# Performance work log

Measured on AMD Instinct MI355X. Metric: run time of the kernel, lower is better.

The kernel has to match this reference:

```python
import jax, jax.numpy as jnp
import numpy as np

N = 10000
E = 160000
NT = 4      # num_types
NB = 8      # bessel basis size
U = 32      # env_embed_multiplicity
R_MAX = 6.0
AVG_NEIGH = 16.0
POLY_P = 6.0


def _mlp(x, Ws):
    # nequip ScalarMLPFunction: no biases, forward-normalized weights, SiLU between layers
    n = len(Ws)
    for i, W in enumerate(Ws):
        x = x @ (W * (1.0 / jnp.sqrt(jnp.float32(W.shape[0]))))
        if i < n - 1:
            x = jax.nn.silu(x)
    return x


def _poly_cutoff(r, rc, p=POLY_P):
    x = r / rc
    out = (1.0 - ((p + 1.0) * (p + 2.0) / 2.0) * x ** p
           + p * (p + 2.0) * x ** (p + 1.0)
           - (p * (p + 1.0) / 2.0) * x ** (p + 2.0))
    return out * (x < 1.0)


def _weighted_channels(edge_attr, w):
    # MakeWeightedChannels: per-edge, per-channel weight for each irrep block
    # edge_attr: [E,4] = (0e | 1o), w: [E,U,2] -> out [E,U,4]
    wd = jnp.concatenate([w[:, :, 0:1], jnp.repeat(w[:, :, 1:2], 3, axis=-1)], axis=-1)
    return edge_attr[:, None, :] * wd


def _forward(edge_index, node_attrs, edge_attr, edge_embed, edge_length,
             W2b0, W2b1, W2b2, Wenv0, Wlat0, Wlat1, Wenv1, Wfin0, Wfin1,
             Wlin_s, Wlin_v, resnet_params):
    n_nodes = node_attrs.shape[0]
    n_edges = edge_attr.shape[0]
    center, neigh = edge_index[0], edge_index[1]
    cut = _poly_cutoff(edge_length, R_MAX)[:, None]           # [E,1], same per-layer cutoff
    env_norm = 1.0 / jnp.sqrt(AVG_NEIGH)
    sqrt3 = jnp.sqrt(3.0)
    c = jnp.exp(resnet_params)                                 # resnet update coefficients

    # ---- two-body latent (layer 0 latent)
    lat_in = jnp.concatenate([node_attrs[center], node_attrs[neigh], edge_embed], axis=-1)
    latents = _mlp(lat_in, [W2b0, W2b1, W2b2]) * cut           # [E,512]
    norm2 = c[0] ** 2
    latents = latents * (c[0] / jnp.sqrt(norm2))

    # env-embed MLP layer 0: feature weights + env weights
    w0 = _mlp(latents, [Wenv0])                                # [E,4U]
    w_feat = w0[:, :2 * U].reshape(n_edges, U, 2)
    w_env = w0[:, 2 * U:].reshape(n_edges, U, 2)
    features = _weighted_channels(edge_attr, w_feat)           # [E,U,4]

    def env_embed_edges(w_env):
        env_w = _weighted_channels(edge_attr, w_env)           # [E,U,4]
        env = jax.ops.segment_sum(env_w, center, num_segments=n_nodes) * env_norm
        return env[center]                                     # [E,U,4]

    # ---- layer 0 TP ('uuu', e3nn component norm): (0e+1o) x (0e+1o) -> [0e,0e,1o,1o]
    env_e = env_embed_edges(w_env)
    t0 = features[:, :, 0] * env_e[:, :, 0]
    t1 = jnp.sum(features[:, :, 1:] * env_e[:, :, 1:], axis=-1) / sqrt3
    v0 = features[:, :, 0:1] * env_e[:, :, 1:]
    v1 = features[:, :, 1:] * env_e[:, :, 0:1]
    scalars = jnp.concatenate([t0, t1], axis=-1)               # [E,2U]
    # e3nn Linear mixing full_out_irreps back to (0e+1o) x U
    alpha = 1.0 / jnp.sqrt(2.0 * U)
    y_s = (scalars @ Wlin_s) * alpha                           # [E,U]
    x_v = jnp.concatenate([v0, v1], axis=1)                    # [E,2U,3]
    y_v = jnp.einsum('ekd,ko->eod', x_v, Wlin_v) * alpha       # [E,U,3]
    features = jnp.concatenate([y_s[..., None], y_v], axis=-1)

    # latent resnet update
    new_lat = _mlp(jnp.concatenate([latents, scalars], axis=-1), [Wlat0, Wlat1]) * cut
    latents = (jnp.sqrt(norm2) * latents + c[1] * new_lat) / jnp.sqrt(norm2 + c[1] ** 2)
    norm2 = norm2 + c[1] ** 2

    w_env = _mlp(latents, [Wenv1]).reshape(n_edges, U, 2)

    # ---- layer 1 TP (last layer): only scalar outputs [0e,0e]
    env_e = env_embed_edges(w_env)
    t0 = features[:, :, 0] * env_e[:, :, 0]
    t1 = jnp.sum(features[:, :, 1:] * env_e[:, :, 1:], axis=-1) / sqrt3
    scalars = jnp.concatenate([t0, t1], axis=-1)               # [E,2U]
    # (the last-layer Linear output features are never used downstream -> skipped)

    # ---- final latent
    new_lat = _mlp(jnp.concatenate([latents, scalars], axis=-1), [Wfin0, Wfin1]) * cut
    latents = (jnp.sqrt(norm2) * latents + c[2] * new_lat) / jnp.sqrt(norm2 + c[2] ** 2)
    return latents                                             # [E,512] edge features


def setup_inputs() -> dict:
    key = jax.random.key(0)
    ks = jax.random.split(key, 20)
    edge_index = jax.random.randint(ks[0], (2, E), 0, N)
    node_types = jax.random.randint(ks[1], (N,), 0, NT)
    node_attrs = jax.nn.one_hot(node_types, NT, dtype=jnp.float32)
    edge_length = jax.random.uniform(ks[2], (E,), minval=0.5, maxval=R_MAX)
    vec = jax.random.normal(ks[3], (E, 3), dtype=jnp.float32)
    unit = vec / jnp.linalg.norm(vec, axis=-1, keepdims=True)
    # component-normalized real spherical harmonics: l=0 -> 1, l=1 -> sqrt(3)*unit
    edge_attr = jnp.concatenate([jnp.ones((E, 1), jnp.float32), jnp.sqrt(3.0) * unit], axis=-1)
    nb = jnp.arange(1, NB + 1, dtype=jnp.float32)
    edge_embed = (jnp.sqrt(2.0 / R_MAX)
                  * jnp.sin(nb[None, :] * jnp.pi * edge_length[:, None] / R_MAX)
                  / edge_length[:, None])
    w = lambda k, shp: jax.random.normal(k, shp, dtype=jnp.float32)
    return {
        'edge_index': edge_index, 'node_attrs': node_attrs, 'edge_attr': edge_attr,
        'edge_embed': edge_embed, 'edge_length': edge_length,
        'W2b0': w(ks[4], (2 * NT + NB, 128)), 'W2b1': w(ks[5], (128, 256)), 'W2b2': w(ks[6], (256, 512)),
        'Wenv0': w(ks[7], (512, 4 * U)),
        'Wlat0': w(ks[8], (512 + 2 * U, 512)), 'Wlat1': w(ks[9], (512, 512)),
        'Wenv1': w(ks[10], (512, 2 * U)),
        'Wfin0': w(ks[11], (512 + 2 * U, 512)), 'Wfin1': w(ks[12], (512, 512)),
        'Wlin_s': w(ks[13], (2 * U, U)), 'Wlin_v': w(ks[14], (2 * U, U)),
        'resnet_params': jnp.zeros((3,), jnp.float32),
    }


def reference(edge_index, node_attrs, edge_attr, edge_embed, edge_length,
              W2b0, W2b1, W2b2, Wenv0, Wlat0, Wlat1, Wenv1, Wfin0, Wfin1,
              Wlin_s, Wlin_v, resnet_params):
    return _forward(edge_index, node_attrs, edge_attr, edge_embed, edge_length,
                    W2b0, W2b1, W2b2, Wenv0, Wlat0, Wlat1, Wenv1, Wfin0, Wfin1,
                    Wlin_s, Wlin_v, resnet_params)
```

## Files before the change

### kernel.cpp

```cpp
#include <hip/hip_runtime.h>
#include <math.h>

#define E_EDGES 160000
#define N_NODES 10000

typedef __attribute__((ext_vector_type(8))) __bf16 bf16x8;
typedef __attribute__((ext_vector_type(4))) float f32x4;
typedef __attribute__((ext_vector_type(4))) unsigned int u32x4;

__device__ __forceinline__ unsigned short f2bf(float x) {
    unsigned u = __float_as_uint(x);
    u += 0x7fff + ((u >> 16) & 1);
    return (unsigned short)(u >> 16);
}
__device__ __forceinline__ float bf2f(unsigned short h) {
    return __uint_as_float(((unsigned)h) << 16);
}
__device__ __forceinline__ float siluf(float v) {
    return v / (1.0f + __expf(-v));
}
__device__ __forceinline__ void gload16(const unsigned short* g, unsigned short* l) {
    __builtin_amdgcn_global_load_lds(
        (const __attribute__((address_space(1))) void*)g,
        (__attribute__((address_space(3))) void*)l, 16, 0, 0);
}

__global__ __launch_bounds__(256)
void prep_kernel(const int* __restrict__ ei, const float* __restrict__ na,
                 const float* __restrict__ embed, const float* __restrict__ elen,
                 float* __restrict__ cut, unsigned short* __restrict__ A16b,
                 int* __restrict__ deg)
{
    int e = blockIdx.x * blockDim.x + threadIdx.x;
    if (e >= E_EDGES) return;
    float r  = elen[e];
    float x  = r * (1.0f / 6.0f);
    float x2 = x * x;
    float x6 = x2 * x2 * x2;
    float c = 1.0f - 28.0f * x6 + 48.0f * x6 * x - 21.0f * x6 * x2;
    cut[e] = (x < 1.0f) ? c : 0.0f;
    int ctr = ei[e];
    int ngh = ei[E_EDGES + e];
    atomicAdd(&deg[ctr], 1);
    float4 ac = *(const float4*)(na + (size_t)ctr * 4);
    float4 an = *(const float4*)(na + (size_t)ngh * 4);
    float4 b0 = *(const float4*)(embed + (size_t)e * 8);
    float4 b1 = *(const float4*)(embed + (size_t)e * 8 + 4);
    unsigned short* o = A16b + (size_t)e * 32;
    o[0]  = f2bf(ac.x); o[1]  = f2bf(ac.y); o[2]  = f2bf(ac.z); o[3]  = f2bf(ac.w);
    o[4]  = f2bf(an.x); o[5]  = f2bf(an.y); o[6]  = f2bf(an.z); o[7]  = f2bf(an.w);
    o[8]  = f2bf(b0.x); o[9]  = f2bf(b0.y); o[10] = f2bf(b0.z); o[11] = f2bf(b0.w);
    o[12] = f2bf(b1.x); o[13] = f2bf(b1.y); o[14] = f2bf(b1.z); o[15] = f2bf(b1.w);
    #pragma unroll
    for (int i = 16; i < 32; ++i) o[i] = 0;
}

__global__ __launch_bounds__(256)
void wtrans_all(const float* __restrict__ w0, const float* __restrict__ w1,
                const float* __restrict__ w2, const float* __restrict__ w3,
                const float* __restrict__ w4, const float* __restrict__ w5,
                const float* __restrict__ w6, const float* __restrict__ w7,
                const float* __restrict__ w8, unsigned short* __restrict__ wbuf)
{
    int blk = blockIdx.x;
    const float* W; int K, N, Kpad, Npad; size_t dbase; int lstart; float sc;
    const float s16  = 0.25f;
    const float s128 = 0.088388347648318447f;
    const float s256 = 0.0625f;
    const float s512 = 0.044194173824159223f;
    const float s576 = 0.041666666666666664f;
    if      (blk <   16) { W=w0; K=16;  N=128; Kpad=32;  Npad=128; dbase=0;       lstart=0;    sc=s16;  }
    else if (blk <  144) { W=w1; K=128; N=256; Kpad=128; Npad=256; dbase=4096;    lstart=16;   sc=s128; }
    else if (blk <  656) { W=w2; K=256; N=512; Kpad=256; Npad=512; dbase=36864;   lstart=144;  sc=s256; }
    else if (blk <  912) { W=w3; K=512; N=128; Kpad=512; Npad=128; dbase=167936;  lstart=656;  sc=s512; }
    else if (blk < 2064) { W=w4; K=576; N=512; Kpad=576; Npad=512; dbase=233472;  lstart=912;  sc=s576; }
    else if (blk < 3088) { W=w5; K=512; N=512; Kpad=512; Npad=512; dbase=528384;  lstart=2064; sc=s512; }
    else if (blk < 3344) { W=w6; K=512; N=64;  Kpad=512; Npad=128; dbase=790528;  lstart=3088; sc=s512; }
    else if (blk < 4496) { W=w7; K=576; N=512; Kpad=576; Npad=512; dbase=856064;  lstart=3344; sc=s576; }
    else                 { W=w8; K=512; N=512; Kpad=512; Npad=512; dbase=1150976; lstart=4496; sc=s512; }
    int local = (blk - lstart) * 256 + threadIdx.x;
    int n = local % Npad, k = local / Npad;
    if (k >= Kpad) return;
    float v = (k < K && n < N) ? W[(size_t)k * N + n] * sc : 0.0f;
    wbuf[dbase + (size_t)n * Kpad + k] = f2bf(v);
}

__global__ __launch_bounds__(1024)
void scan_kernel(const int* __restrict__ deg, int* __restrict__ offs)
{
    __shared__ int part[1024];
    int t = threadIdx.x;
    int base = t * 10;
    int loc[10];
    int s = 0;
    #pragma unroll
    for (int i = 0; i < 10; ++i) {
        int idx = base + i;
        int d = (idx < N_NODES) ? deg[idx] : 0;
        loc[i] = s; s += d;
    }
    part[t] = s;
    __syncthreads();
    for (int o = 1; o < 1024; o <<= 1) {
        int v = (t >= o) ? part[t - o] : 0;
        __syncthreads();
        part[t] += v;
        __syncthreads();
    }
    int excl = (t > 0) ? part[t - 1] : 0;
    #pragma unroll
    for (int i = 0; i < 10; ++i) {
        int idx = base + i;
        if (idx < N_NODES) offs[idx] = excl + loc[i];
    }
    if (t == 1023) offs[N_NODES] = part[1023];
}

__global__ __launch_bounds__(256)
void fill_kernel(const int* __restrict__ ei, const int* __restrict__ offs,
                 int* __restrict__ cnt, int* __restrict__ elist)
{
    int e = blockIdx.x * blockDim.x + threadIdx.x;
    if (e >= E_EDGES) return;
    int c = ei[e];
    int pos = offs[c] + atomicAdd(&cnt[c], 1);
    elist[pos] = e;
}

__global__ __launch_bounds__(256)
void sortseg_kernel(const int* __restrict__ offs, int* __restrict__ elist)
{
    int node = blockIdx.x * 4 + (threadIdx.x >> 6);
    int l = threadIdx.x & 63;
    if (node >= N_NODES) return;
    int b = offs[node], en = offs[node + 1];
    int deg = en - b;
    if (deg <= 1) return;
    if (deg <= 64) {
        int v = (l < deg) ? elist[b + l] : 0x7fffffff;
        #pragma unroll
        for (int k = 2; k <= 64; k <<= 1) {
            #pragma unroll
            for (int j = k >> 1; j > 0; j >>= 1) {
                int o = __shfl_xor(v, j);
                bool dirUp = ((l & k) == 0);
                bool lower = ((l & j) == 0);
                int mn = v < o ? v : o;
                int mx = v < o ? o : v;
                v = (dirUp == lower) ? mn : mx;
            }
        }
        if (l < deg) elist[b + l] = v;
    } else if (l == 0) {
        for (int i = b + 1; i < en; ++i) {
            int v = elist[i];
            int j = i - 1;
            while (j >= b && elist[j] > v) { elist[j + 1] = elist[j]; --j; }
            elist[j + 1] = v;
        }
    }
}

__global__ __launch_bounds__(256)
void envgather_kernel(const unsigned short* __restrict__ Wb, int wstride, int woff,
                      const float* __restrict__ ea, const int* __restrict__ offs,
                      const int* __restrict__ elist, float* __restrict__ env)
{
    int n = blockIdx.x * 2 + (threadIdx.x >> 7);
    int t = threadIdx.x & 127;
    if (n >= N_NODES) return;
    int u = t >> 2, comp = t & 3;
    int widx = woff + u * 2 + (comp ? 1 : 0);
    int beg = offs[n], end = offs[n + 1];
    float acc = 0.0f;
    for (int i = beg; i < end; ++i) {
        int e = elist[i];
        float w = bf2f(Wb[(size_t)e * wstride + widx]);
        float a = ea[(size_t)e * 4 + comp];
        acc += a * w;
    }
    env[(size_t)n * 128 + t] = acc * 0.25f;
}

template<int EPIL>
__global__ __launch_bounds__(256)
void gemm_bf16(const unsigned short* __restrict__ A1,
               int K, const unsigned short* __restrict__ Bt,
               int nx, int ldc, int Nstore,
               unsigned short* __restrict__ Cb)
{
    __shared__ __align__(16) unsigned short SB[3][2][128 * 32];
    const int tid  = threadIdx.x;
    const int lane = tid & 63;
    const int wid  = tid >> 6;
    const int wr   = wid >> 1, wc = wid & 1;
    const int nwg = gridDim.x;
    const int fid = blockIdx.x;
    const int q = nwg >> 3, r = nwg & 7;
    const int xcd = fid & 7, j = fid >> 3;
    const int L = ((xcd < r) ? xcd * (q + 1) : r * (q + 1) + (xcd - r) * q) + j;
    const int bn = (L % nx) * 128;
    const int bm = (L / nx) * 128;

    const int l15 = lane & 15;
    const int l4r = lane >> 2;
    const int sk8 = (((lane & 3) ^ ((lane >> 3) & 3)) << 3);
    const int rk8 = ((((lane >> 4) ^ ((l15 >> 1) & 3)) & 3) << 3);
    const int T   = K >> 5;

    f32x4 acc[4][4] = {};

    auto stage = [&](int t, int b) {
        int k0 = t << 5;
        #pragma unroll
        for (int i = 0; i < 2; ++i) {
            int ch  = (wid << 1) + i;
            int row = (ch << 4) + l4r;
            gload16(A1 + (size_t)(bm + row) * K + k0 + sk8, &SB[b][0][ch << 9]);
            gload16(Bt + (size_t)(bn + row) * K + k0 + sk8, &SB[b][1][ch << 9]);
        }
    };

    stage(0, 0);
    if (T >= 2) stage(1, 1);

    for (int t = 0; t < T; ++t) {
        if (t < T - 1) asm volatile("s_waitcnt vmcnt(4)" ::: "memory");
        else           asm volatile("s_waitcnt vmcnt(0)" ::: "memory");
        __builtin_amdgcn_s_barrier();
        __builtin_amdgcn_sched_barrier(0);

        if (t + 2 < T) stage(t + 2, (t + 2) % 3);

        const unsigned short* As = &SB[t % 3][0][0];
        const unsigned short* Bs = &SB[t % 3][1][0];
        bf16x8 af[4], bfr[4];
        #pragma unroll
        for (int m = 0; m < 4; ++m)
            af[m] = __builtin_bit_cast(bf16x8, *(const u32x4*)&As[(wr * 64 + m * 16 + l15) * 32 + rk8]);
        #pragma unroll
        for (int n = 0; n < 4; ++n)
            bfr[n] = __builtin_bit_cast(bf16x8, *(const u32x4*)&Bs[(wc * 64 + n * 16 + l15) * 32 + rk8]);

        __builtin_amdgcn_s_setprio(1);
        #pragma unroll
        for (int m = 0; m < 4; ++m)
            #pragma unroll
            for (int n = 0; n < 4; ++n)
                acc[m][n] = __builtin_amdgcn_mfma_f32_16x16x32_bf16(af[m], bfr[n], acc[m][n], 0, 0, 0);
        __builtin_amdgcn_s_setprio(0);

        asm volatile("s_waitcnt lgkmcnt(0)" ::: "memory");
        __builtin_amdgcn_sched_barrier(0);
    }

    #pragma unroll
    for (int m = 0; m < 4; ++m) {
        int rbase = bm + wr * 64 + m * 16 + ((lane >> 4) << 2);
        #pragma unroll
        for (int n = 0; n < 4; ++n) {
            int col = bn + wc * 64 + n * 16 + l15;
            if (col < Nstore) {
                #pragma unroll
                for (int rr = 0; rr < 4; ++rr) {
                    int row = rbase + rr;
                    Cb[(size_t)row * ldc + col] = f2bf(acc[m][n][rr]);
                }
            }
        }
    }
}

__global__ __launch_bounds__(512)
void mlp2b(const unsigned short* __restrict__ A16b,
           const unsigned short* __restrict__ W0t,
           const unsigned short* __restrict__ W1t,
           const unsigned short* __restrict__ W2t,
           const float* __restrict__ cut, unsigned short* __restrict__ Lb)
{
    __shared__ __align__(16) unsigned short SA[64 * 32];
    __shared__ __align__(16) unsigned short H1[64 * 128];
    __shared__ __align__(16) unsigned short H2[64 * 256];
    const int tid  = threadIdx.x;
    const int lane = tid & 63;
    const int wid  = tid >> 6;
    const int l15  = lane & 15;
    const int l4r  = lane >> 2;
    const int lk8  = (lane >> 4) << 3;
    const int sk8  = (((lane & 3) ^ ((lane >> 3) & 3)) << 3);
    const int rk8  = ((((lane >> 4) ^ ((l15 >> 1) & 3)) & 3) << 3);
    const int bm   = blockIdx.x * 64;
    const int hrow4 = (lane >> 4) << 2;

    if (wid < 4) {
        int row = (wid << 4) + l4r;
        gload16(A16b + (size_t)(bm + row) * 32 + sk8, &SA[wid << 9]);
    }
    asm volatile("s_waitcnt vmcnt(0)" ::: "memory");
    __builtin_amdgcn_s_barrier();
    __builtin_amdgcn_sched_barrier(0);

    {
        int hc = wid * 16 + l15;
        bf16x8 wf = __builtin_bit_cast(bf16x8, *(const u32x4*)(W0t + (size_t)hc * 32 + lk8));
        #pragma unroll
        for (int mi = 0; mi < 4; ++mi) {
            bf16x8 af = __builtin_bit_cast(bf16x8, *(const u32x4*)&SA[(mi * 16 + l15) * 32 + rk8]);
            f32x4 a = {};
            a = __builtin_amdgcn_mfma_f32_16x16x32_bf16(af, wf, a, 0, 0, 0);
            #pragma unroll
            for (int rr = 0; rr < 4; ++rr) {
                int er = mi * 16 + hrow4 + rr;
                H1[er * 128 + (((hc >> 3) ^ (er & 7)) << 3) + (hc & 7)] = f2bf(siluf(a[rr]));
            }
        }
    }
    asm volatile("s_waitcnt lgkmcnt(0)" ::: "memory");
    __builtin_amdgcn_s_barrier();
    __builtin_amdgcn_sched_barrier(0);

    {
        f32x4 acc[4][2] = {};
        #pragma unroll
        for (int kt = 0; kt < 4; ++kt) {
            bf16x8 hf[4], wf[2];
            #pragma unroll
            for (int fa = 0; fa < 4; ++fa) {
                int er = fa * 16 + l15;
                int slotp = (kt * 4 + (lane >> 4)) ^ (er & 7);
                hf[fa] = __builtin_bit_cast(bf16x8, *(const u32x4*)&H1[er * 128 + slotp * 8]);
            }
            #pragma unroll
            for (int fb = 0; fb < 2; ++fb) {
                int hc = wid * 32 + fb * 16 + l15;
                wf[fb] = __builtin_bit_cast(bf16x8, *(const u32x4*)(W1t + (size_t)hc * 128 + kt * 32 + lk8));
            }
            #pragma unroll
            for (int fa = 0; fa < 4; ++fa)
                #pragma unroll
                for (int fb = 0; fb < 2; ++fb)
                    acc[fa][fb] = __builtin_amdgcn_mfma_f32_16x16x32_bf16(hf[fa], wf[fb], acc[fa][fb], 0, 0, 0);
        }
        asm volatile("s_waitcnt lgkmcnt(0)" ::: "memory");
        __builtin_amdgcn_s_barrier();
        #pragma unroll
        for (int fa = 0; fa < 4; ++fa)
            #pragma unroll
            for (int fb = 0; fb < 2; ++fb)
                #pragma unroll
                for (int rr = 0; rr < 4; ++rr) {
                    int er = fa * 16 + hrow4 + rr;
                    int hc = wid * 32 + fb * 16 + l15;
                    H2[er * 256 + (((hc >> 3) ^ (er & 7)) << 3) + (hc & 7)] = f2bf(siluf(acc[fa][fb][rr]));
                }
    }
    asm volatile("s_waitcnt lgkmcnt(0)" ::: "memory");
    __builtin_amdgcn_s_barrier();
    __builtin_amdgcn_sched_barrier(0);

    f32x4 acc[4][4] = {};
    #pragma unroll 1
    for (int kt = 0; kt < 8; ++kt) {
        bf16x8 hf[4], wf[4];
        #pragma unroll
        for (int fa = 0; fa < 4; ++fa) {
            int er = fa * 16 + l15;
            int slotp = (kt * 4 + (lane >> 4)) ^ (er & 7);
            hf[fa] = __builtin_bit_cast(bf16x8, *(const u32x4*)&H2[er * 256 + slotp * 8]);
        }
        #pragma unroll
        for (int fb = 0; fb < 4; ++fb) {
            int oc = wid * 64 + fb * 16 + l15;
            wf[fb] = __builtin_bit_cast(bf16x8, *(const u32x4*)(W2t + (size_t)oc * 256 + kt * 32 + lk8));
        }
        __builtin_amdgcn_s_setprio(1);
        #pragma unroll
        for (int fa = 0; fa < 4; ++fa)
            #pragma unroll
            for (int fb = 0; fb < 4; ++fb)
                acc[fa][fb] = __builtin_amdgcn_mfma_f32_16x16x32_bf16(hf[fa], wf[fb], acc[fa][fb], 0, 0, 0);
        __builtin_amdgcn_s_setprio(0);
    }
    #pragma unroll
    for (int fa = 0; fa < 4; ++fa) {
        int rbase = bm + fa * 16 + hrow4;
        #pragma unroll
        for (int fb = 0; fb < 4; ++fb) {
            int col = wid * 64 + fb * 16 + l15;
            #pragma unroll
            for (int rr = 0; rr < 4; ++rr) {
                int row = rbase + rr;
                Lb[(size_t)row * 512 + col] = f2bf(acc[fa][fb][rr] * cut[row]);
            }
        }
    }
}

template<int EPIL2>
__global__ __launch_bounds__(512)
void fused_mlp(const unsigned short* __restrict__ A1,
               const unsigned short* __restrict__ A2,
               const unsigned short* __restrict__ W1t,
               const unsigned short* __restrict__ W2t,
               float* __restrict__ Cf, unsigned short* __restrict__ Cb,
               const float* __restrict__ cut, const float* __restrict__ rp)
{
    __shared__ __align__(16) unsigned short Hl[128 * 512];
    __shared__ __align__(16) unsigned short SA[3][128 * 32];
    const int tid  = threadIdx.x;
    const int lane = tid & 63;
    const int wid  = tid >> 6;
    const int l15  = lane & 15;
    const int l4r  = lane >> 2;
    const int lk8  = (lane >> 4) << 3;
    const int sk8  = (((lane & 3) ^ ((lane >> 3) & 3)) << 3);
    const int rk8  = ((((lane >> 4) ^ ((l15 >> 1) & 3)) & 3) << 3);
    const int bm   = blockIdx.x * 128;
    const int hcol0 = wid * 64;
    const int ocol0 = wid * 64;

    auto stage = [&](int t, int b) {
        int k0 = t << 5;
        int row = (wid << 4) + l4r;
        const unsigned short* gp;
        if (k0 < 512) gp = A1 + (size_t)(bm + row) * 512 + k0 + sk8;
        else          gp = A2 + (size_t)(bm + row) * 64 + (k0 - 512) + sk8;
        gload16(gp, &SA[b][wid << 9]);
    };

    f32x4 acc1[8][4] = {};
    stage(0, 0);
    stage(1, 1);

    for (int t = 0; t < 18; ++t) {
        __builtin_amdgcn_sched_barrier(0);
        if (t < 17) asm volatile("s_waitcnt vmcnt(1)" ::: "memory");
        else        asm volatile("s_waitcnt vmcnt(0)" ::: "memory");
        __builtin_amdgcn_s_barrier();
        __builtin_amdgcn_sched_barrier(0);

        const unsigned short* As = &SA[t % 3][0];
        int k0 = t << 5;
        bf16x8 af[8], wf[4];
        #pragma unroll
        for (int mi = 0; mi < 8; ++mi)
            af[mi] = __builtin_bit_cast(bf16x8, *(const u32x4*)&As[(mi * 16 + l15) * 32 + rk8]);
        #pragma unroll
        for (int ni = 0; ni < 4; ++ni) {
            int hc = hcol0 + ni * 16 + l15;
            wf[ni] = __builtin_bit_cast(bf16x8, *(const u32x4*)(W1t + (size_t)hc * 576 + k0 + lk8));
        }
        __builtin_amdgcn_sched_barrier(0);
        if (t + 2 < 18) stage(t + 2, (t + 2) % 3);
        __builtin_amdgcn_sched_barrier(0);
        asm volatile("s_waitcnt lgkmcnt(0)" ::: "memory");
        __builtin_amdgcn_sched_barrier(0);

        __builtin_amdgcn_s_setprio(1);
        #pragma unroll
        for (int mi = 0; mi < 8; ++mi)
            #pragma unroll
            for (int ni = 0; ni < 4; ++ni)
                acc1[mi][ni] = __builtin_amdgcn_mfma_f32_16x16x32_bf16(af[mi], wf[ni], acc1[mi][ni], 0, 0, 0);
        __builtin_amdgcn_s_setprio(0);
    }

    #pragma unroll
    for (int mi = 0; mi < 8; ++mi)
        #pragma unroll
        for (int ni = 0; ni < 4; ++ni)
            #pragma unroll
            for (int rr = 0; rr < 4; ++rr) {
                int er = mi * 16 + ((lane >> 4) << 2) + rr;
                int hc = hcol0 + ni * 16 + l15;
                float v = acc1[mi][ni][rr];
                v = v / (1.0f + __expf(-v));
                int slotp = (hc >> 3) ^ (er & 7);
                Hl[er * 512 + slotp * 8 + (hc & 7)] = f2bf(v);
            }
    asm volatile("s_waitcnt lgkmcnt(0)" ::: "memory");
    __builtin_amdgcn_s_barrier();
    __builtin_amdgcn_sched_barrier(0);

    f32x4 acc2[8][4] = {};
    #pragma unroll 1
    for (int kt = 0; kt < 16; ++kt) {
        bf16x8 hf[8], w2f[4];
        #pragma unroll
        for (int fa = 0; fa < 8; ++fa) {
            int er = fa * 16 + l15;
            int slotp = (kt * 4 + (lane >> 4)) ^ (er & 7);
            hf[fa] = __builtin_bit_cast(bf16x8, *(const u32x4*)&Hl[er * 512 + slotp * 8]);
        }
        #pragma unroll
        for (int fb = 0; fb < 4; ++fb) {
            int oc = ocol0 + fb * 16 + l15;
            w2f[fb] = __builtin_bit_cast(bf16x8, *(const u32x4*)(W2t + (size_t)oc * 512 + kt * 32 + lk8));
        }
        __builtin_amdgcn_s_setprio(1);
        #pragma unroll
        for (int fa = 0; fa < 8; ++fa)
            #pragma unroll
            for (int fb = 0; fb < 4; ++fb)
                acc2[fa][fb] = __builtin_amdgcn_mfma_f32_16x16x32_bf16(hf[fa], w2f[fb], acc2[fa][fb], 0, 0, 0);
        __builtin_amdgcn_s_setprio(0);
    }

    float c0 = __expf(rp[0]), c1 = __expf(rp[1]), c2 = __expf(rp[2]);
    #pragma unroll
    for (int fa = 0; fa < 8; ++fa) {
        int rbase = bm + fa * 16 + ((lane >> 4) << 2);
        #pragma unroll
        for (int fb = 0; fb < 4; ++fb) {
            int col = ocol0 + fb * 16 + l15;
            #pragma unroll
            for (int rr = 0; rr < 4; ++rr) {
                int row = rbase + rr;
                float v = acc2[fa][fb][rr];
                size_t off2 = (size_t)row * 512 + col;
                if (EPIL2 == 3) {
                    float old = bf2f(Cb[off2]);
                    v = (c0 * old + c1 * v * cut[row]) * rsqrtf(c0 * c0 + c1 * c1);
                    Cb[off2] = f2bf(v);
                } else {
                    float old = bf2f(Cb[off2]);
                    float n2 = c0 * c0 + c1 * c1;
                    v = (sqrtf(n2) * old + c2 * v * cut[row]) * rsqrtf(n2 + c2 * c2);
                    Cf[off2] = v;
                }
            }
        }
    }
}

__global__ __launch_bounds__(256)
void tp0_kernel(const unsigned short* __restrict__ W0b, const float* __restrict__ ea,
                const float* __restrict__ env, const int* __restrict__ ei,
                const float* __restrict__ Ws, const float* __restrict__ Wv,
                unsigned short* __restrict__ scalb, unsigned short* __restrict__ feat2b)
{
    __shared__ float sc[8][64];
    __shared__ float xv[8][64][3];
    __shared__ float Wsl[2048];
    __shared__ float Wvl[2048];
    int tid = threadIdx.x;
    const float alpha = 0.125f;
    #pragma unroll
    for (int i = 0; i < 8; ++i) {
        Wsl[tid + i * 256] = Ws[tid + i * 256] * alpha;
        Wvl[tid + i * 256] = Wv[tid + i * 256] * alpha;
    }
    int le = tid >> 5;
    int u  = tid & 31;
    int e  = blockIdx.x * 8 + le;
    int c  = ei[e];
    float4 a = *(const float4*)(ea + (size_t)e * 4);
    const float* ep = env + (size_t)c * 128 + u * 4;
    float e0 = ep[0], e1 = ep[1], e2 = ep[2], e3 = ep[3];
    float wf0 = bf2f(W0b[(size_t)e * 128 + u * 2]);
    float wf1 = bf2f(W0b[(size_t)e * 128 + u * 2 + 1]);
    float f0 = a.x * wf0;
    float f1 = a.y * wf1, f2 = a.z * wf1, f3 = a.w * wf1;
    const float rs3 = 0.57735026918962576f;
    float t0 = f0 * e0;
    float t1 = (f1 * e1 + f2 * e2 + f3 * e3) * rs3;
    scalb[(size_t)e * 64 + u]      = f2bf(t0);
    scalb[(size_t)e * 64 + 32 + u] = f2bf(t1);
    sc[le][u]      = t0;
    sc[le][32 + u] = t1;
    xv[le][u][0] = f0 * e1; xv[le][u][1] = f0 * e2; xv[le][u][2] = f0 * e3;
    xv[le][32 + u][0] = f1 * e0; xv[le][32 + u][1] = f2 * e0; xv[le][32 + u][2] = f3 * e0;
    __syncthreads();
    float ys = 0.0f, yv0 = 0.0f, yv1 = 0.0f, yv2 = 0.0f;
    #pragma unroll 8
    for (int k = 0; k < 64; ++k) {
        float ws = Wsl[k * 32 + u];
        float wv = Wvl[k * 32 + u];
        ys  = fmaf(sc[le][k], ws, ys);
        yv0 = fmaf(xv[le][k][0], wv, yv0);
        yv1 = fmaf(xv[le][k][1], wv, yv1);
        yv2 = fmaf(xv[le][k][2], wv, yv2);
    }
    ushort4 ov;
    ov.x = f2bf(ys);
    ov.y = f2bf(yv0);
    ov.z = f2bf(yv1);
    ov.w = f2bf(yv2);
    *(ushort4*)(feat2b + (size_t)e * 128 + u * 4) = ov;
}

__global__ __launch_bounds__(256)
void tp1_kernel(const unsigned short* __restrict__ feat2b, const float* __restrict__ env,
                const int* __restrict__ ei, unsigned short* __restrict__ scalb)
{
    int idx = blockIdx.x * blockDim.x + threadIdx.x;
    if (idx >= E_EDGES * 32) return;
    int e = idx >> 5, u = idx & 31;
    int c = ei[e];
    const float* ep = env + (size_t)c * 128 + u * 4;
    ushort4 f4 = *(const ushort4*)(feat2b + (size_t)e * 128 + u * 4);
    float fx = bf2f(f4.x), fy = bf2f(f4.y), fz = bf2f(f4.z), fw = bf2f(f4.w);
    const float rs3 = 0.57735026918962576f;
    float t0 = fx * ep[0];
    float t1 = (fy * ep[1] + fz * ep[2] + fw * ep[3]) * rs3;
    scalb[(size_t)e * 64 + u]      = f2bf(t0);
    scalb[(size_t)e * 64 + 32 + u] = f2bf(t1);
}

extern "C" void kernel_launch(void* const* d_in, const int* in_sizes, int n_in,
                              void* d_out, int out_size, void* d_ws, size_t ws_size,
                              hipStream_t stream)
{
    const int*   ei     = (const int*)d_in[0];
    const float* na     = (const float*)d_in[1];
    const float* ea     = (const float*)d_in[2];
    const float* embed  = (const float*)d_in[3];
    const float* elen   = (const float*)d_in[4];
    const float* W2b0   = (const float*)d_in[5];
    const float* W2b1   = (const float*)d_in[6];
    const float* W2b2   = (const float*)d_in[7];
    const float* Wenv0  = (const float*)d_in[8];
    const float* Wlat0  = (const float*)d_in[9];
    const float* Wlat1  = (const float*)d_in[10];
    const float* Wenv1  = (const float*)d_in[11];
    const float* Wfin0  = (const float*)d_in[12];
    const float* Wfin1  = (const float*)d_in[13];
    const float* Wlin_s = (const float*)d_in[14];
    const float* Wlin_v = (const float*)d_in[15];
    const float* rp     = (const float*)d_in[16];

    float* L = (float*)d_out;
    const size_t E = E_EDGES;

    char* ws = (char*)d_ws;
    size_t off = 0;
    auto alloc = [&](size_t b) { void* p = ws + off; off += (b + 255) & ~(size_t)255; return p; };
    float*          cutb   = (float*)alloc(E * 4);
    unsigned short* wbuf   = (unsigned short*)alloc((size_t)1413120 * 2);
    float*          envb   = (float*)alloc((size_t)N_NODES * 128 * 4);
    unsigned short* scalb  = (unsigned short*)alloc(E * 64 * 2);
    unsigned short* feat2b = (unsigned short*)alloc(E * 128 * 2);
    unsigned short* Lb     = (unsigned short*)alloc(E * 512 * 2);
    int*            degcnt = (int*)alloc((size_t)2 * N_NODES * 4);
    int*            offs   = (int*)alloc((N_NODES + 1) * 4);
    int*            elist  = (int*)alloc(E * 4);
    unsigned short* A16b   = (unsigned short*)alloc(E * 32 * 2);
    unsigned short* R1b    = (unsigned short*)alloc(E * 128 * 2);
    unsigned short* WE1b   = (unsigned short*)alloc(E * 64 * 2);
    int* deg = degcnt;
    int* cnt = degcnt + N_NODES;

    unsigned short* W2b0t  = wbuf;
    unsigned short* W2b1t  = wbuf + 4096;
    unsigned short* W2b2t  = wbuf + 36864;
    unsigned short* Wenv0t = wbuf + 167936;
    unsigned short* Wlat0t = wbuf + 233472;
    unsigned short* Wlat1t = wbuf + 528384;
    unsigned short* Wenv1t = wbuf + 790528;
    unsigned short* Wfin0t = wbuf + 856064;
    unsigned short* Wfin1t = wbuf + 1150976;
    wtrans_all<<<5520, 256, 0, stream>>>(W2b0, W2b1, W2b2, Wenv0, Wlat0, Wlat1,
                                         Wenv1, Wfin0, Wfin1, wbuf);

    hipMemsetAsync(degcnt, 0, (size_t)2 * N_NODES * 4, stream);
    prep_kernel<<<E_EDGES / 256, 256, 0, stream>>>(ei, na, embed, elen, cutb, A16b, deg);
    scan_kernel<<<1, 1024, 0, stream>>>(deg, offs);
    fill_kernel<<<E_EDGES / 256, 256, 0, stream>>>(ei, offs, cnt, elist);
    sortseg_kernel<<<N_NODES / 4, 256, 0, stream>>>(offs, elist);

    mlp2b<<<2500, 512, 0, stream>>>(A16b, W2b0t, W2b1t, W2b2t, cutb, Lb);

    gemm_bf16<0><<<1250, 256, 0, stream>>>(Lb, 512, Wenv0t, 1, 128, 128, R1b);

    envgather_kernel<<<N_NODES / 2, 256, 0, stream>>>(R1b, 128, 64, ea, offs, elist, envb);
    tp0_kernel<<<E_EDGES / 8, 256, 0, stream>>>(R1b, ea, envb, ei, Wlin_s, Wlin_v, scalb, feat2b);

    fused_mlp<3><<<1250, 512, 0, stream>>>(Lb, scalb, Wlat0t, Wlat1t, nullptr, Lb, cutb, rp);

    gemm_bf16<0><<<1250, 256, 0, stream>>>(Lb, 512, Wenv1t, 1, 64, 64, WE1b);

    envgather_kernel<<<N_NODES / 2, 256, 0, stream>>>(WE1b, 64, 0, ea, offs, elist, envb);
    tp1_kernel<<<E_EDGES * 32 / 256, 256, 0, stream>>>(feat2b, envb, ei, scalb);

    fused_mlp<4><<<1250, 512, 0, stream>>>(Lb, scalb, Wfin0t, Wfin1t, L, Lb, cutb, rp);
}
```

Before: 1.077 ms.

## Stage first-layer weight tiles into LDS via async loads in fused MLP

The first GEMM of the fused two-layer MLP used to read W1 fragments straight from global memory on every k-step. It now copies each W1 k-tile into LDS alongside the activation tile with global_load_lds, reusing the idle hidden-activation buffer as a triple-buffered staging area, and waits on a deeper vmcnt. This swaps per-wave global weight loads for shared async copies, which hides their latency inside the pipeline. The cost is more LDS traffic and an extra barrier before the hidden buffer is overwritten.

```diff
diff --git a/kernel.cpp b/kernel.cpp
--- a/kernel.cpp
+++ b/kernel.cpp
@@ -416,10 +416,10 @@
     const int sk8  = (((lane & 3) ^ ((lane >> 3) & 3)) << 3);
     const int rk8  = ((((lane >> 4) ^ ((l15 >> 1) & 3)) & 3) << 3);
     const int bm   = blockIdx.x * 128;
-    const int hcol0 = wid * 64;
-    const int ocol0 = wid * 64;
-
-    auto stage = [&](int t, int b) {
+    const int col0 = wid * 64;
+    const int hrow4 = (lane >> 4) << 2;
+
+    auto stageA = [&](int t, int b) {
         int k0 = t << 5;
         int row = (wid << 4) + l4r;
         const unsigned short* gp;
@@ -427,32 +427,37 @@
         else          gp = A2 + (size_t)(bm + row) * 64 + (k0 - 512) + sk8;
         gload16(gp, &SA[b][wid << 9]);
     };
+    auto stageW = [&](int t, int b) {
+        int k0 = t << 5;
+        #pragma unroll
+        for (int i = 0; i < 4; ++i) {
+            int ch  = (wid << 2) + i;
+            int row = (ch << 4) + l4r;
+            gload16(W1t + (size_t)row * 576 + k0 + sk8, &Hl[b * 16384 + (ch << 9)]);
+        }
+    };
 
     f32x4 acc1[8][4] = {};
-    stage(0, 0);
-    stage(1, 1);
+    stageA(0, 0); stageW(0, 0);
+    stageA(1, 1); stageW(1, 1);
 
     for (int t = 0; t < 18; ++t) {
-        __builtin_amdgcn_sched_barrier(0);
-        if (t < 17) asm volatile("s_waitcnt vmcnt(1)" ::: "memory");
+        if (t < 17) asm volatile("s_waitcnt vmcnt(5)" ::: "memory");
         else        asm volatile("s_waitcnt vmcnt(0)" ::: "memory");
         __builtin_amdgcn_s_barrier();
         __builtin_amdgcn_sched_barrier(0);
 
+        if (t + 2 < 18) { stageA(t + 2, (t + 2) % 3); stageW(t + 2, (t + 2) % 3); }
+
         const unsigned short* As = &SA[t % 3][0];
-        int k0 = t << 5;
+        const unsigned short* Ws = &Hl[(t % 3) * 16384];
         bf16x8 af[8], wf[4];
         #pragma unroll
         for (int mi = 0; mi < 8; ++mi)
             af[mi] = __builtin_bit_cast(bf16x8, *(const u32x4*)&As[(mi * 16 + l15) * 32 + rk8]);
         #pragma unroll
-        for (int ni = 0; ni < 4; ++ni) {
-            int hc = hcol0 + ni * 16 + l15;
-            wf[ni] = __builtin_bit_cast(bf16x8, *(const u32x4*)(W1t + (size_t)hc * 576 + k0 + lk8));
-        }
-        __builtin_amdgcn_sched_barrier(0);
-        if (t + 2 < 18) stage(t + 2, (t + 2) % 3);
-        __builtin_amdgcn_sched_barrier(0);
+        for (int ni = 0; ni < 4; ++ni)
+            wf[ni] = __builtin_bit_cast(bf16x8, *(const u32x4*)&Ws[(col0 + ni * 16 + l15) * 32 + rk8]);
         asm volatile("s_waitcnt lgkmcnt(0)" ::: "memory");
         __builtin_amdgcn_sched_barrier(0);
 
@@ -464,6 +469,8 @@
                 acc1[mi][ni] = __builtin_amdgcn_mfma_f32_16x16x32_bf16(af[mi], wf[ni], acc1[mi][ni], 0, 0, 0);
         __builtin_amdgcn_s_setprio(0);
     }
+    __builtin_amdgcn_s_barrier();
+    __builtin_amdgcn_sched_barrier(0);
 
     #pragma unroll
     for (int mi = 0; mi < 8; ++mi)
@@ -471,12 +478,9 @@
         for (int ni = 0; ni < 4; ++ni)
             #pragma unroll
             for (int rr = 0; rr < 4; ++rr) {
-                int er = mi * 16 + ((lane >> 4) << 2) + rr;
-                int hc = hcol0 + ni * 16 + l15;
-                float v = acc1[mi][ni][rr];
-                v = v / (1.0f + __expf(-v));
-                int slotp = (hc >> 3) ^ (er & 7);
-                Hl[er * 512 + slotp * 8 + (hc & 7)] = f2bf(v);
+                int er = mi * 16 + hrow4 + rr;
+                int hc = col0 + ni * 16 + l15;
+                Hl[er * 512 + (((hc >> 3) ^ (er & 7)) << 3) + (hc & 7)] = f2bf(siluf(acc1[mi][ni][rr]));
             }
     asm volatile("s_waitcnt lgkmcnt(0)" ::: "memory");
     __builtin_amdgcn_s_barrier();
@@ -494,7 +498,7 @@
         }
         #pragma unroll
         for (int fb = 0; fb < 4; ++fb) {
-            int oc = ocol0 + fb * 16 + l15;
+            int oc = col0 + fb * 16 + l15;
             w2f[fb] = __builtin_bit_cast(bf16x8, *(const u32x4*)(W2t + (size_t)oc * 512 + kt * 32 + lk8));
         }
         __builtin_amdgcn_s_setprio(1);
@@ -509,10 +513,10 @@
     float c0 = __expf(rp[0]), c1 = __expf(rp[1]), c2 = __expf(rp[2]);
     #pragma unroll
     for (int fa = 0; fa < 8; ++fa) {
-        int rbase = bm + fa * 16 + ((lane >> 4) << 2);
+        int rbase = bm + fa * 16 + hrow4;
         #pragma unroll
         for (int fb = 0; fb < 4; ++fb) {
-            int col = ocol0 + fb * 16 + l15;
+            int col = col0 + fb * 16 + l15;
             #pragma unroll
             for (int rr = 0; rr < 4; ++rr) {
                 int row = rbase + rr;
```

Result: no change. 1.071 ms (-0.5%).
